# Kernel optimization log

Hardware: AMD Instinct MI355X
Metric: run time of the kernel (lower is better)

The kernel has to match this reference:

```python
import jax, jax.numpy as jnp
import numpy as np

# Instant-NGP style multi-resolution hash grid (torch-ngp convention)
NUM_LEVELS = 32
LEVEL_DIM = 2
LOG2_T = 19
T = 1 << LOG2_T            # per-level hash table size (power of two)
BASE_RES = 1
PER_LEVEL_SCALE = 2.0
PRIMES = (1, 2654435761, 805459861)  # spatial hash primes (uint32, wraps)
# 8 corner offsets of the unit cube, [8, 3]
OFFSETS_NP = np.array([[(c >> d) & 1 for d in range(3)] for c in range(8)], dtype=np.uint32)


def hash_encode(x, embeddings):
    """x: [N,3] in [0,1); embeddings: [L, T, F] -> [N, L*F]."""
    offsets = jnp.asarray(OFFSETS_NP)                       # [8,3] uint32
    offs_f = offsets.astype(x.dtype)                        # [8,3]
    feats = []
    for l in range(NUM_LEVELS):
        scale = float(np.exp2(l * np.log2(PER_LEVEL_SCALE)) * BASE_RES - 1.0)
        res = int(np.ceil(scale)) + 1
        pos = x * jnp.float32(scale) + 0.5                  # [N,3]
        pos0 = jnp.floor(pos)
        frac = pos - pos0                                   # [N,3] in [0,1)
        pg = pos0.astype(jnp.uint32)                        # [N,3]
        corners = pg[:, None, :] + offsets[None, :, :]      # [N,8,3] uint32
        if res ** 3 <= T:
            # dense (non-colliding) linear index at coarse levels
            r = jnp.uint32(res)
            idx = corners[..., 0] + corners[..., 1] * r + corners[..., 2] * (r * r)
        else:
            # spatial hash: xor of coordinate * prime (uint32 wraparound)
            idx = (corners[..., 0] * jnp.uint32(PRIMES[0])
                   ^ corners[..., 1] * jnp.uint32(PRIMES[1])
                   ^ corners[..., 2] * jnp.uint32(PRIMES[2]))
        idx = (idx & jnp.uint32(T - 1)).astype(jnp.int32)   # [N,8]
        f = embeddings[l][idx]                              # gather -> [N,8,F]
        # trilinear interpolation weights
        w = jnp.prod(jnp.where(offs_f[None] == 1, frac[:, None, :], 1.0 - frac[:, None, :]), axis=-1)  # [N,8]
        feats.append(jnp.sum(f * w[..., None], axis=1))     # [N,F]
    return jnp.concatenate(feats, axis=-1)                  # [N, L*F]


def setup_inputs() -> dict:
    key = jax.random.key(0)
    k = jax.random.split(key, 5)
    N = 1 << 20
    x = jax.random.uniform(k[0], (N, 3), dtype=jnp.float32)
    embeddings = jax.random.normal(k[1], (NUM_LEVELS, T, LEVEL_DIM), dtype=jnp.float32) * 1e-2
    in_dim = NUM_LEVELS * LEVEL_DIM  # 64
    W1 = jax.random.normal(k[2], (in_dim, 128), dtype=jnp.float32) * (1.0 / np.sqrt(in_dim))
    b1 = jnp.zeros((128,), jnp.float32)
    W2 = jax.random.normal(k[3], (128, 128), dtype=jnp.float32) * (1.0 / np.sqrt(128))
    b2 = jnp.zeros((128,), jnp.float32)
    W3 = jax.random.normal(k[4], (128, 1), dtype=jnp.float32) * (1.0 / np.sqrt(128))
    b3 = jnp.zeros((1,), jnp.float32)
    return {"x": x, "embeddings": embeddings, "W1": W1, "b1": b1, "W2": W2, "b2": b2, "W3": W3, "b3": b3}


def reference(x, embeddings, W1, b1, W2, b2, W3, b3):
    h = hash_encode(x, embeddings)                 # [N, 64]
    h = jax.nn.relu(h @ W1 + b1)                   # [N, 128]
    h = jax.nn.relu(h @ W2 + b2)                   # [N, 128]
    return h @ W3 + b3                             # [N, 1]
```

## Files before the change

kernel.cpp:

```cpp
#include <hip/hip_runtime.h>
#include <stdint.h>


#define NLV 32
#define LOG2T 19
#define TSZ (1u << LOG2T)
#define TMASK (TSZ - 1u)
#define PRIME2 2654435761u
#define PRIME3 805459861u

typedef float v2f __attribute__((ext_vector_type(2)));
typedef float f32x4 __attribute__((ext_vector_type(4)));
typedef float f32x4u __attribute__((ext_vector_type(4), aligned(8)));
typedef short bf16x8 __attribute__((ext_vector_type(8)));
typedef uint32_t u32x4 __attribute__((ext_vector_type(4)));
typedef uint32_t u32x2 __attribute__((ext_vector_type(2)));

__device__ __forceinline__ uint32_t pack_bf16(float a, float b) {
  uint32_t ua = __float_as_uint(a), ub = __float_as_uint(b);
  ua = (ua + 0x7fffu + ((ua >> 16) & 1u)) >> 16;
  ub = (ub + 0x7fffu + ((ub >> 16) & 1u)) >> 16;
  return ua | (ub << 16);
}
__device__ __forceinline__ uint16_t bf16_rne(float a) {
  uint32_t u = __float_as_uint(a);
  u = (u + 0x7fffu + ((u >> 16) & 1u)) >> 16;
  return (uint16_t)u;
}

__global__ __launch_bounds__(256) void encode_kernel(
    const float* __restrict__ x, const float* __restrict__ emb,
    uint32_t* __restrict__ feats, int offset, int count, int chunkCap, int bpl)
{
  const int bid = (int)blockIdx.x;
  const int xcd = bid & 7;
  const int j = bid >> 3;
  const int phase = j / bpl;
  const int within = j - phase * bpl;
  const int l = xcd + (phase << 3);

  const float scale = (float)((double)(1ULL << l) - 1.0);
  const uint32_t r = 1u << l, rr = r * r;
  const bool dense = (l <= 6);
  const v2f* __restrict__ embl = (const v2f*)(emb + ((size_t)l << (LOG2T + 1)));

  #pragma unroll
  for (int k = 0; k < 4; ++k) {
    int li = within * 1024 + k * 256 + (int)threadIdx.x;
    if (li < count) {
      int p = offset + li;
      float xv = __builtin_nontemporal_load(&x[3 * p + 0]);
      float yv = __builtin_nontemporal_load(&x[3 * p + 1]);
      float zv = __builtin_nontemporal_load(&x[3 * p + 2]);
      float px = __fadd_rn(__fmul_rn(xv, scale), 0.5f);
      float py = __fadd_rn(__fmul_rn(yv, scale), 0.5f);
      float pz = __fadd_rn(__fmul_rn(zv, scale), 0.5f);
      float bx = floorf(px), by = floorf(py), bz = floorf(pz);
      float fx = __fsub_rn(px, bx), fy = __fsub_rn(py, by), fz = __fsub_rn(pz, bz);
      uint32_t gx = (uint32_t)bx, gy = (uint32_t)by, gz = (uint32_t)bz;
      float wx0 = __fsub_rn(1.0f, fx), wx1 = fx;
      float wy0 = __fsub_rn(1.0f, fy), wy1 = fy;
      float wz0 = __fsub_rn(1.0f, fz), wz1 = fz;

      float f0 = 0.0f, f1 = 0.0f;
      #pragma unroll
      for (int cp = 0; cp < 4; ++cp) {
        uint32_t cy = gy + (uint32_t)(cp & 1);
        uint32_t cz = gz + (uint32_t)(cp >> 1);
        float wyz = __fmul_rn((cp & 1) ? wy1 : wy0, (cp >> 1) ? wz1 : wz0);
        v2f e0, e1;
        if (dense) {
          uint32_t i0 = gx + cy * r + cz * rr;
          f32x4 e2 = *(const f32x4u*)&embl[i0];
          e0[0] = e2.x; e0[1] = e2.y; e1[0] = e2.z; e1[1] = e2.w;
        } else {
          uint32_t h = (cy * PRIME2) ^ (cz * PRIME3);
          uint32_t i0 = (gx ^ h) & TMASK;
          if (!(gx & 1u)) {
            f32x4 e2 = *(const f32x4*)&embl[i0 & ~1u];
            bool odd = (i0 & 1u) != 0u;
            e0[0] = odd ? e2.z : e2.x; e0[1] = odd ? e2.w : e2.y;
            e1[0] = odd ? e2.x : e2.z; e1[1] = odd ? e2.y : e2.w;
          } else {
            uint32_t i1 = ((gx + 1u) ^ h) & TMASK;
            e0 = embl[i0];
            e1 = embl[i1];
          }
        }
        float w0 = __fmul_rn(wx0, wyz), w1 = __fmul_rn(wx1, wyz);
        f0 = fmaf(w0, e0[0], f0); f1 = fmaf(w0, e0[1], f1);
        f0 = fmaf(w1, e1[0], f0); f1 = fmaf(w1, e1[1], f1);
      }
      __builtin_nontemporal_store(pack_bf16(f0, f1),
                                  &feats[(size_t)l * (size_t)chunkCap + li]);
    }
  }
}

__global__ __launch_bounds__(512) void prep_kernel(
    const float* __restrict__ W1, const float* __restrict__ W2,
    uint16_t* __restrict__ wimg)
{
  int i = (int)blockIdx.x * 512 + (int)threadIdx.x;
  if (i < 8192) {
    int k = i >> 7, n = i & 127;
    wimg[(n * 128 + ((k * 2) ^ ((n & 7) << 4))) >> 1] = bf16_rne(W1[i]);
  } else if (i < 24576) {
    int t = i - 8192;
    int k = t >> 7, n = t & 127;
    wimg[(16384 + n * 256 + ((k * 2) ^ ((n & 7) << 4))) >> 1] = bf16_rne(W2[t]);
  }
}

#define MLP_G 64

__global__ __launch_bounds__(256, 1) void mlp_kernel(
    const uint32_t* __restrict__ feats, const uint16_t* __restrict__ wimg,
    const float* __restrict__ b1, const float* __restrict__ b2,
    const float* __restrict__ W3, const float* __restrict__ b3,
    float* __restrict__ out, int offset, int count, int chunkCap, int nGroups)
{
  __shared__ char lds[24576];
  char* xb = lds;
  char* hb = lds + 8192;

  const int tid = (int)threadIdx.x;
  const int lane = tid & 63;
  const int w = tid >> 6;
  const int col = lane & 15;
  const int kh = lane >> 4;
  const char* wbytes = (const char*)wimg;

  bf16x8 w1f[2][8], w2f[4][8];
  #pragma unroll
  for (int nt = 0; nt < 8; ++nt) {
    int n = nt * 16 + col;
    #pragma unroll
    for (int kt = 0; kt < 2; ++kt)
      w1f[kt][nt] = *(const bf16x8*)(wbytes + n * 128 +
                        ((kt * 64 + kh * 16) ^ ((n & 7) << 4)));
    #pragma unroll
    for (int q = 0; q < 4; ++q)
      w2f[q][nt] = *(const bf16x8*)(wbytes + 16384 + n * 256 +
                        ((q * 64 + kh * 16) ^ ((n & 7) << 4)));
  }
  float bias1r[8][4];
  #pragma unroll
  for (int nt = 0; nt < 8; ++nt)
    #pragma unroll
    for (int rg = 0; rg < 4; ++rg)
      bias1r[nt][rg] = b1[nt * 16 + kh * 4 + rg];
  float bias2[8], w3v[8];
  #pragma unroll
  for (int nt = 0; nt < 8; ++nt) {
    bias2[nt] = b2[nt * 16 + col];
    w3v[nt] = W3[nt * 16 + col];
  }
  const float b3v = b3[0];

  const int pp = w * 16 + col;
  const int sp = tid & 63;
  const int sq = tid >> 6;

  int g = (int)blockIdx.x;
  u32x4 xr0, xr1;
  {
    int src = g * MLP_G + sp; if (src >= count) src = 0;
    int pl = sq * 8;
    xr0.x = __builtin_nontemporal_load(&feats[(size_t)(pl + 0) * chunkCap + src]);
    xr0.y = __builtin_nontemporal_load(&feats[(size_t)(pl + 1) * chunkCap + src]);
    xr0.z = __builtin_nontemporal_load(&feats[(size_t)(pl + 2) * chunkCap + src]);
    xr0.w = __builtin_nontemporal_load(&feats[(size_t)(pl + 3) * chunkCap + src]);
    xr1.x = __builtin_nontemporal_load(&feats[(size_t)(pl + 4) * chunkCap + src]);
    xr1.y = __builtin_nontemporal_load(&feats[(size_t)(pl + 5) * chunkCap + src]);
    xr1.z = __builtin_nontemporal_load(&feats[(size_t)(pl + 6) * chunkCap + src]);
    xr1.w = __builtin_nontemporal_load(&feats[(size_t)(pl + 7) * chunkCap + src]);
  }

  for (; g < nGroups; g += (int)gridDim.x) {
    *(u32x4*)(xb + sp * 128 + ((sq * 32 +  0) ^ ((sp & 7) << 4))) = xr0;
    *(u32x4*)(xb + sp * 128 + ((sq * 32 + 16) ^ ((sp & 7) << 4))) = xr1;
    __syncthreads();

    {
      int gn = g + (int)gridDim.x; if (gn >= nGroups) gn = g;
      int src = gn * MLP_G + sp; if (src >= count) src = 0;
      int pl = sq * 8;
      xr0.x = __builtin_nontemporal_load(&feats[(size_t)(pl + 0) * chunkCap + src]);
      xr0.y = __builtin_nontemporal_load(&feats[(size_t)(pl + 1) * chunkCap + src]);
      xr0.z = __builtin_nontemporal_load(&feats[(size_t)(pl + 2) * chunkCap + src]);
      xr0.w = __builtin_nontemporal_load(&feats[(size_t)(pl + 3) * chunkCap + src]);
      xr1.x = __builtin_nontemporal_load(&feats[(size_t)(pl + 4) * chunkCap + src]);
      xr1.y = __builtin_nontemporal_load(&feats[(size_t)(pl + 5) * chunkCap + src]);
      xr1.z = __builtin_nontemporal_load(&feats[(size_t)(pl + 6) * chunkCap + src]);
      xr1.w = __builtin_nontemporal_load(&feats[(size_t)(pl + 7) * chunkCap + src]);
    }

    bf16x8 xa[2];
    #pragma unroll
    for (int kt = 0; kt < 2; ++kt)
      xa[kt] = *(const bf16x8*)(xb + pp * 128 +
                   ((kt * 64 + kh * 16) ^ ((pp & 7) << 4)));
    f32x4 acc[8];
    #pragma unroll
    for (int nt = 0; nt < 8; ++nt) acc[nt] = {0.f, 0.f, 0.f, 0.f};
    #pragma unroll
    for (int kt = 0; kt < 2; ++kt)
      #pragma unroll
      for (int nt = 0; nt < 8; ++nt)
        acc[nt] = __builtin_amdgcn_mfma_f32_16x16x32_bf16(
                      w1f[kt][nt], xa[kt], acc[nt], 0, 0, 0);

    #pragma unroll
    for (int nt = 0; nt < 8; ++nt) {
      uint32_t lo = pack_bf16(fmaxf(acc[nt][0] + bias1r[nt][0], 0.0f),
                              fmaxf(acc[nt][1] + bias1r[nt][1], 0.0f));
      uint32_t hi = pack_bf16(fmaxf(acc[nt][2] + bias1r[nt][2], 0.0f),
                              fmaxf(acc[nt][3] + bias1r[nt][3], 0.0f));
      u32x2 v; v.x = lo; v.y = hi;
      *(u32x2*)(hb + pp * 256 + ((nt * 32 + kh * 8) ^ ((pp & 7) << 4))) = v;
    }
    __syncthreads();

    f32x4 acc2[8];
    #pragma unroll
    for (int nt = 0; nt < 8; ++nt) acc2[nt] = {0.f, 0.f, 0.f, 0.f};
    #pragma unroll
    for (int q = 0; q < 4; ++q) {
      bf16x8 ha = *(const bf16x8*)(hb + pp * 256 +
                      ((q * 64 + kh * 16) ^ ((pp & 7) << 4)));
      #pragma unroll
      for (int nt = 0; nt < 8; ++nt)
        acc2[nt] = __builtin_amdgcn_mfma_f32_16x16x32_bf16(
                       ha, w2f[q][nt], acc2[nt], 0, 0, 0);
    }

    float osum[4] = {0.f, 0.f, 0.f, 0.f};
    #pragma unroll
    for (int nt = 0; nt < 8; ++nt) {
      #pragma unroll
      for (int rg = 0; rg < 4; ++rg)
        osum[rg] = fmaf(fmaxf(acc2[nt][rg] + bias2[nt], 0.0f), w3v[nt], osum[rg]);
    }
    #pragma unroll
    for (int rg = 0; rg < 4; ++rg) {
      osum[rg] += __shfl_xor(osum[rg], 1);
      osum[rg] += __shfl_xor(osum[rg], 2);
      osum[rg] += __shfl_xor(osum[rg], 4);
      osum[rg] += __shfl_xor(osum[rg], 8);
    }
    const int base = g * MLP_G;
    #pragma unroll
    for (int rg = 0; rg < 4; ++rg) {
      if (col == rg) {
        int pr = base + w * 16 + kh * 4 + rg;
        if (pr < count) out[offset + pr] = osum[rg] + b3v;
      }
    }
  }
}

extern "C" void kernel_launch(void* const* d_in, const int* in_sizes, int n_in,
                              void* d_out, int out_size, void* d_ws, size_t ws_size,
                              hipStream_t stream) {
  const float* x   = (const float*)d_in[0];
  const float* emb = (const float*)d_in[1];
  const float* W1  = (const float*)d_in[2];
  const float* b1  = (const float*)d_in[3];
  const float* W2  = (const float*)d_in[4];
  const float* b2  = (const float*)d_in[5];
  const float* W3  = (const float*)d_in[6];
  const float* b3  = (const float*)d_in[7];
  float* out = (float*)d_out;
  const int N = in_sizes[0] / 3;

  uint16_t* wimg = (uint16_t*)d_ws;
  uint32_t* feats = (uint32_t*)((char*)d_ws + 49152);
  const size_t perPoint = (size_t)NLV * sizeof(uint32_t);
  size_t avail = (ws_size > 49152) ? ws_size - 49152 : 0;
  size_t capz = avail / perPoint;
  if (capz > (size_t)N) capz = (size_t)N;
  int cap = (int)capz & ~1023;
  if (cap <= 0) cap = (N < 1024) ? N : 1024;

  prep_kernel<<<48, 512, 0, stream>>>(W1, W2, wimg);

  for (int off = 0; off < N; off += cap) {
    int cnt = (N - off < cap) ? (N - off) : cap;
    int bpl = (cnt + 1023) / 1024;
    encode_kernel<<<32 * bpl, 256, 0, stream>>>(x, emb, feats, off, cnt, cap, bpl);
    int nGroups = (cnt + MLP_G - 1) / MLP_G;
    int nb = nGroups < 2048 ? nGroups : 2048;
    mlp_kernel<<<nb, 256, 0, stream>>>(
        feats, wimg, b1, b2, W3, b3, out, off, cnt, cap, nGroups);
  }
}
```

Baseline: 1.056 ms.

## Fuse hash encoding and MLP into a single per-block kernel

Replaces the separate level-major encode kernel and persistent MLP kernel with one kernel. Each 64-point block computes all 32 level features straight into LDS and then runs the two MFMA layers and the output dot product. This removes the global round trip of the intermediate feature buffer, the chunking loop and one kernel launch. In exchange, the level-major schedule that kept one level's table slice hot in cache is lost, since all levels are now gathered concurrently. Weights are also re-read from memory per block instead of staying in registers across a persistent loop.

```diff
diff --git a/kernel.cpp b/kernel.cpp
--- a/kernel.cpp
+++ b/kernel.cpp
@@ -1,5 +1,6 @@
 #include <hip/hip_runtime.h>
 #include <stdint.h>
+#include <math.h>
 
 
 #define NLV 32
@@ -16,6 +17,8 @@
 typedef uint32_t u32x4 __attribute__((ext_vector_type(4)));
 typedef uint32_t u32x2 __attribute__((ext_vector_type(2)));
 
+struct Scales { float s[NLV]; };
+
 __device__ __forceinline__ uint32_t pack_bf16(float a, float b) {
   uint32_t ua = __float_as_uint(a), ub = __float_as_uint(b);
   ua = (ua + 0x7fffu + ((ua >> 16) & 1u)) >> 16;
@@ -26,75 +29,6 @@
   uint32_t u = __float_as_uint(a);
   u = (u + 0x7fffu + ((u >> 16) & 1u)) >> 16;
   return (uint16_t)u;
-}
-
-__global__ __launch_bounds__(256) void encode_kernel(
-    const float* __restrict__ x, const float* __restrict__ emb,
-    uint32_t* __restrict__ feats, int offset, int count, int chunkCap, int bpl)
-{
-  const int bid = (int)blockIdx.x;
-  const int xcd = bid & 7;
-  const int j = bid >> 3;
-  const int phase = j / bpl;
-  const int within = j - phase * bpl;
-  const int l = xcd + (phase << 3);
-
-  const float scale = (float)((double)(1ULL << l) - 1.0);
-  const uint32_t r = 1u << l, rr = r * r;
-  const bool dense = (l <= 6);
-  const v2f* __restrict__ embl = (const v2f*)(emb + ((size_t)l << (LOG2T + 1)));
-
-  #pragma unroll
-  for (int k = 0; k < 4; ++k) {
-    int li = within * 1024 + k * 256 + (int)threadIdx.x;
-    if (li < count) {
-      int p = offset + li;
-      float xv = __builtin_nontemporal_load(&x[3 * p + 0]);
-      float yv = __builtin_nontemporal_load(&x[3 * p + 1]);
-      float zv = __builtin_nontemporal_load(&x[3 * p + 2]);
-      float px = __fadd_rn(__fmul_rn(xv, scale), 0.5f);
-      float py = __fadd_rn(__fmul_rn(yv, scale), 0.5f);
-      float pz = __fadd_rn(__fmul_rn(zv, scale), 0.5f);
-      float bx = floorf(px), by = floorf(py), bz = floorf(pz);
-      float fx = __fsub_rn(px, bx), fy = __fsub_rn(py, by), fz = __fsub_rn(pz, bz);
-      uint32_t gx = (uint32_t)bx, gy = (uint32_t)by, gz = (uint32_t)bz;
-      float wx0 = __fsub_rn(1.0f, fx), wx1 = fx;
-      float wy0 = __fsub_rn(1.0f, fy), wy1 = fy;
-      float wz0 = __fsub_rn(1.0f, fz), wz1 = fz;
-
-      float f0 = 0.0f, f1 = 0.0f;
-      #pragma unroll
-      for (int cp = 0; cp < 4; ++cp) {
-        uint32_t cy = gy + (uint32_t)(cp & 1);
-        uint32_t cz = gz + (uint32_t)(cp >> 1);
-        float wyz = __fmul_rn((cp & 1) ? wy1 : wy0, (cp >> 1) ? wz1 : wz0);
-        v2f e0, e1;
-        if (dense) {
-          uint32_t i0 = gx + cy * r + cz * rr;
-          f32x4 e2 = *(const f32x4u*)&embl[i0];
-          e0[0] = e2.x; e0[1] = e2.y; e1[0] = e2.z; e1[1] = e2.w;
-        } else {
-          uint32_t h = (cy * PRIME2) ^ (cz * PRIME3);
-          uint32_t i0 = (gx ^ h) & TMASK;
-          if (!(gx & 1u)) {
-            f32x4 e2 = *(const f32x4*)&embl[i0 & ~1u];
-            bool odd = (i0 & 1u) != 0u;
-            e0[0] = odd ? e2.z : e2.x; e0[1] = odd ? e2.w : e2.y;
-            e1[0] = odd ? e2.x : e2.z; e1[1] = odd ? e2.y : e2.w;
-          } else {
-            uint32_t i1 = ((gx + 1u) ^ h) & TMASK;
-            e0 = embl[i0];
-            e1 = embl[i1];
-          }
-        }
-        float w0 = __fmul_rn(wx0, wyz), w1 = __fmul_rn(wx1, wyz);
-        f0 = fmaf(w0, e0[0], f0); f1 = fmaf(w0, e0[1], f1);
-        f0 = fmaf(w1, e1[0], f0); f1 = fmaf(w1, e1[1], f1);
-      }
-      __builtin_nontemporal_store(pack_bf16(f0, f1),
-                                  &feats[(size_t)l * (size_t)chunkCap + li]);
-    }
-  }
 }
 
 __global__ __launch_bounds__(512) void prep_kernel(
@@ -112,150 +46,167 @@
   }
 }
 
-#define MLP_G 64
-
-__global__ __launch_bounds__(256, 1) void mlp_kernel(
-    const uint32_t* __restrict__ feats, const uint16_t* __restrict__ wimg,
+__device__ __forceinline__ uint32_t encode_level(
+    float scale, uint32_t r, bool dense, const v2f* __restrict__ embl,
+    float xv, float yv, float zv)
+{
+  float px = __fadd_rn(__fmul_rn(xv, scale), 0.5f);
+  float py = __fadd_rn(__fmul_rn(yv, scale), 0.5f);
+  float pz = __fadd_rn(__fmul_rn(zv, scale), 0.5f);
+  float bx = floorf(px), by = floorf(py), bz = floorf(pz);
+  float fx = __fsub_rn(px, bx), fy = __fsub_rn(py, by), fz = __fsub_rn(pz, bz);
+  uint32_t gx = (uint32_t)bx, gy = (uint32_t)by, gz = (uint32_t)bz;
+  float wx0 = __fsub_rn(1.0f, fx), wx1 = fx;
+  float wy0 = __fsub_rn(1.0f, fy), wy1 = fy;
+  float wz0 = __fsub_rn(1.0f, fz), wz1 = fz;
+  const uint32_t rr = r * r;
+
+  float f0 = 0.0f, f1 = 0.0f;
+  #pragma unroll
+  for (int cp = 0; cp < 4; ++cp) {
+    uint32_t cy = gy + (uint32_t)(cp & 1);
+    uint32_t cz = gz + (uint32_t)(cp >> 1);
+    float wyz = __fmul_rn((cp & 1) ? wy1 : wy0, (cp >> 1) ? wz1 : wz0);
+    v2f e0, e1;
+    if (dense) {
+      uint32_t i0 = gx + cy * r + cz * rr;
+      f32x4 e2 = *(const f32x4u*)&embl[i0];
+      e0[0] = e2.x; e0[1] = e2.y; e1[0] = e2.z; e1[1] = e2.w;
+    } else {
+      uint32_t h = (cy * PRIME2) ^ (cz * PRIME3);
+      uint32_t i0 = (gx ^ h) & TMASK;
+      if (!(gx & 1u)) {
+        f32x4 e2 = *(const f32x4*)&embl[i0 & ~1u];
+        bool odd = (i0 & 1u) != 0u;
+        e0[0] = odd ? e2.z : e2.x; e0[1] = odd ? e2.w : e2.y;
+        e1[0] = odd ? e2.x : e2.z; e1[1] = odd ? e2.y : e2.w;
+      } else {
+        uint32_t i1 = ((gx + 1u) ^ h) & TMASK;
+        e0 = embl[i0];
+        e1 = embl[i1];
+      }
+    }
+    float w0 = __fmul_rn(wx0, wyz), w1 = __fmul_rn(wx1, wyz);
+    f0 = fmaf(w0, e0[0], f0); f1 = fmaf(w0, e0[1], f1);
+    f0 = fmaf(w1, e1[0], f0); f1 = fmaf(w1, e1[1], f1);
+  }
+  return pack_bf16(f0, f1);
+}
+
+__global__ __launch_bounds__(256) void fused_kernel(
+    const float* __restrict__ x, const float* __restrict__ emb,
+    const uint16_t* __restrict__ wimg,
     const float* __restrict__ b1, const float* __restrict__ b2,
     const float* __restrict__ W3, const float* __restrict__ b3,
-    float* __restrict__ out, int offset, int count, int chunkCap, int nGroups)
+    float* __restrict__ out, int count, Scales sc)
 {
   __shared__ char lds[24576];
   char* xb = lds;
   char* hb = lds + 8192;
 
   const int tid = (int)threadIdx.x;
+  const int sp = tid & 63;
+  const int sq = tid >> 6;
+  const int base = (int)blockIdx.x * 64;
+
+  {
+    int gp = base + sp;
+    int src = (gp < count) ? gp : 0;
+    float xv = x[3 * src + 0], yv = x[3 * src + 1], zv = x[3 * src + 2];
+    const int l0 = __builtin_amdgcn_readfirstlane(sq * 8);
+    uint32_t f[8];
+    #pragma unroll
+    for (int i = 0; i < 8; ++i) {
+      const int l = l0 + i;
+      const float scale = sc.s[l];
+      const uint32_t r = 1u << l;
+      const bool dense = (l <= 6);
+      const v2f* embl = (const v2f*)(emb + ((size_t)l << (LOG2T + 1)));
+      f[i] = encode_level(scale, r, dense, embl, xv, yv, zv);
+    }
+    u32x4 v0, v1;
+    v0.x = f[0]; v0.y = f[1]; v0.z = f[2]; v0.w = f[3];
+    v1.x = f[4]; v1.y = f[5]; v1.z = f[6]; v1.w = f[7];
+    int sw = (sp & 7) << 4;
+    *(u32x4*)(xb + sp * 128 + ((sq * 32 +  0) ^ sw)) = v0;
+    *(u32x4*)(xb + sp * 128 + ((sq * 32 + 16) ^ sw)) = v1;
+  }
+  __syncthreads();
+
   const int lane = tid & 63;
   const int w = tid >> 6;
   const int col = lane & 15;
   const int kh = lane >> 4;
+  const int pp = w * 16 + col;
   const char* wbytes = (const char*)wimg;
 
-  bf16x8 w1f[2][8], w2f[4][8];
+  bf16x8 xa[2];
+  #pragma unroll
+  for (int kt = 0; kt < 2; ++kt)
+    xa[kt] = *(const bf16x8*)(xb + pp * 128 +
+                 ((kt * 64 + kh * 16) ^ ((pp & 7) << 4)));
+  f32x4 acc[8];
+  #pragma unroll
+  for (int nt = 0; nt < 8; ++nt) acc[nt] = {0.f, 0.f, 0.f, 0.f};
+  #pragma unroll
+  for (int kt = 0; kt < 2; ++kt)
+    #pragma unroll
+    for (int nt = 0; nt < 8; ++nt) {
+      int n = nt * 16 + col;
+      bf16x8 wf = *(const bf16x8*)(wbytes + n * 128 +
+                      ((kt * 64 + kh * 16) ^ ((n & 7) << 4)));
+      acc[nt] = __builtin_amdgcn_mfma_f32_16x16x32_bf16(wf, xa[kt], acc[nt], 0, 0, 0);
+    }
+
   #pragma unroll
   for (int nt = 0; nt < 8; ++nt) {
-    int n = nt * 16 + col;
-    #pragma unroll
-    for (int kt = 0; kt < 2; ++kt)
-      w1f[kt][nt] = *(const bf16x8*)(wbytes + n * 128 +
-                        ((kt * 64 + kh * 16) ^ ((n & 7) << 4)));
-    #pragma unroll
-    for (int q = 0; q < 4; ++q)
-      w2f[q][nt] = *(const bf16x8*)(wbytes + 16384 + n * 256 +
-                        ((q * 64 + kh * 16) ^ ((n & 7) << 4)));
-  }
-  float bias1r[8][4];
-  #pragma unroll
-  for (int nt = 0; nt < 8; ++nt)
+    f32x4u bias = *(const f32x4u*)(b1 + nt * 16 + kh * 4);
+    uint32_t lo = pack_bf16(fmaxf(acc[nt][0] + bias.x, 0.0f),
+                            fmaxf(acc[nt][1] + bias.y, 0.0f));
+    uint32_t hi = pack_bf16(fmaxf(acc[nt][2] + bias.z, 0.0f),
+                            fmaxf(acc[nt][3] + bias.w, 0.0f));
+    u32x2 v; v.x = lo; v.y = hi;
+    *(u32x2*)(hb + pp * 256 + ((nt * 32 + kh * 8) ^ ((pp & 7) << 4))) = v;
+  }
+
+  f32x4 acc2[8];
+  #pragma unroll
+  for (int nt = 0; nt < 8; ++nt) acc2[nt] = {0.f, 0.f, 0.f, 0.f};
+  #pragma unroll
+  for (int q = 0; q < 4; ++q) {
+    bf16x8 ha = *(const bf16x8*)(hb + pp * 256 +
+                    ((q * 64 + kh * 16) ^ ((pp & 7) << 4)));
+    #pragma unroll
+    for (int nt = 0; nt < 8; ++nt) {
+      int n = nt * 16 + col;
+      bf16x8 wf = *(const bf16x8*)(wbytes + 16384 + n * 256 +
+                      ((q * 64 + kh * 16) ^ ((n & 7) << 4)));
+      acc2[nt] = __builtin_amdgcn_mfma_f32_16x16x32_bf16(ha, wf, acc2[nt], 0, 0, 0);
+    }
+  }
+
+  float osum[4] = {0.f, 0.f, 0.f, 0.f};
+  #pragma unroll
+  for (int nt = 0; nt < 8; ++nt) {
+    float bias = b2[nt * 16 + col];
+    float w3v = W3[nt * 16 + col];
     #pragma unroll
     for (int rg = 0; rg < 4; ++rg)
-      bias1r[nt][rg] = b1[nt * 16 + kh * 4 + rg];
-  float bias2[8], w3v[8];
-  #pragma unroll
-  for (int nt = 0; nt < 8; ++nt) {
-    bias2[nt] = b2[nt * 16 + col];
-    w3v[nt] = W3[nt * 16 + col];
+      osum[rg] = fmaf(fmaxf(acc2[nt][rg] + bias, 0.0f), w3v, osum[rg]);
+  }
+  #pragma unroll
+  for (int rg = 0; rg < 4; ++rg) {
+    osum[rg] += __shfl_xor(osum[rg], 1);
+    osum[rg] += __shfl_xor(osum[rg], 2);
+    osum[rg] += __shfl_xor(osum[rg], 4);
+    osum[rg] += __shfl_xor(osum[rg], 8);
   }
   const float b3v = b3[0];
-
-  const int pp = w * 16 + col;
-  const int sp = tid & 63;
-  const int sq = tid >> 6;
-
-  int g = (int)blockIdx.x;
-  u32x4 xr0, xr1;
-  {
-    int src = g * MLP_G + sp; if (src >= count) src = 0;
-    int pl = sq * 8;
-    xr0.x = __builtin_nontemporal_load(&feats[(size_t)(pl + 0) * chunkCap + src]);
-    xr0.y = __builtin_nontemporal_load(&feats[(size_t)(pl + 1) * chunkCap + src]);
-    xr0.z = __builtin_nontemporal_load(&feats[(size_t)(pl + 2) * chunkCap + src]);
-    xr0.w = __builtin_nontemporal_load(&feats[(size_t)(pl + 3) * chunkCap + src]);
-    xr1.x = __builtin_nontemporal_load(&feats[(size_t)(pl + 4) * chunkCap + src]);
-    xr1.y = __builtin_nontemporal_load(&feats[(size_t)(pl + 5) * chunkCap + src]);
-    xr1.z = __builtin_nontemporal_load(&feats[(size_t)(pl + 6) * chunkCap + src]);
-    xr1.w = __builtin_nontemporal_load(&feats[(size_t)(pl + 7) * chunkCap + src]);
-  }
-
-  for (; g < nGroups; g += (int)gridDim.x) {
-    *(u32x4*)(xb + sp * 128 + ((sq * 32 +  0) ^ ((sp & 7) << 4))) = xr0;
-    *(u32x4*)(xb + sp * 128 + ((sq * 32 + 16) ^ ((sp & 7) << 4))) = xr1;
-    __syncthreads();
-
-    {
-      int gn = g + (int)gridDim.x; if (gn >= nGroups) gn = g;
-      int src = gn * MLP_G + sp; if (src >= count) src = 0;
-      int pl = sq * 8;
-      xr0.x = __builtin_nontemporal_load(&feats[(size_t)(pl + 0) * chunkCap + src]);
-      xr0.y = __builtin_nontemporal_load(&feats[(size_t)(pl + 1) * chunkCap + src]);
-      xr0.z = __builtin_nontemporal_load(&feats[(size_t)(pl + 2) * chunkCap + src]);
-      xr0.w = __builtin_nontemporal_load(&feats[(size_t)(pl + 3) * chunkCap + src]);
-      xr1.x = __builtin_nontemporal_load(&feats[(size_t)(pl + 4) * chunkCap + src]);
-      xr1.y = __builtin_nontemporal_load(&feats[(size_t)(pl + 5) * chunkCap + src]);
-      xr1.z = __builtin_nontemporal_load(&feats[(size_t)(pl + 6) * chunkCap + src]);
-      xr1.w = __builtin_nontemporal_load(&feats[(size_t)(pl + 7) * chunkCap + src]);
-    }
-
-    bf16x8 xa[2];
-    #pragma unroll
-    for (int kt = 0; kt < 2; ++kt)
-      xa[kt] = *(const bf16x8*)(xb + pp * 128 +
-                   ((kt * 64 + kh * 16) ^ ((pp & 7) << 4)));
-    f32x4 acc[8];
-    #pragma unroll
-    for (int nt = 0; nt < 8; ++nt) acc[nt] = {0.f, 0.f, 0.f, 0.f};
-    #pragma unroll
-    for (int kt = 0; kt < 2; ++kt)
-      #pragma unroll
-      for (int nt = 0; nt < 8; ++nt)
-        acc[nt] = __builtin_amdgcn_mfma_f32_16x16x32_bf16(
-                      w1f[kt][nt], xa[kt], acc[nt], 0, 0, 0);
-
-    #pragma unroll
-    for (int nt = 0; nt < 8; ++nt) {
-      uint32_t lo = pack_bf16(fmaxf(acc[nt][0] + bias1r[nt][0], 0.0f),
-                              fmaxf(acc[nt][1] + bias1r[nt][1], 0.0f));
-      uint32_t hi = pack_bf16(fmaxf(acc[nt][2] + bias1r[nt][2], 0.0f),
-                              fmaxf(acc[nt][3] + bias1r[nt][3], 0.0f));
-      u32x2 v; v.x = lo; v.y = hi;
-      *(u32x2*)(hb + pp * 256 + ((nt * 32 + kh * 8) ^ ((pp & 7) << 4))) = v;
-    }
-    __syncthreads();
-
-    f32x4 acc2[8];
-    #pragma unroll
-    for (int nt = 0; nt < 8; ++nt) acc2[nt] = {0.f, 0.f, 0.f, 0.f};
-    #pragma unroll
-    for (int q = 0; q < 4; ++q) {
-      bf16x8 ha = *(const bf16x8*)(hb + pp * 256 +
-                      ((q * 64 + kh * 16) ^ ((pp & 7) << 4)));
-      #pragma unroll
-      for (int nt = 0; nt < 8; ++nt)
-        acc2[nt] = __builtin_amdgcn_mfma_f32_16x16x32_bf16(
-                       ha, w2f[q][nt], acc2[nt], 0, 0, 0);
-    }
-
-    float osum[4] = {0.f, 0.f, 0.f, 0.f};
-    #pragma unroll
-    for (int nt = 0; nt < 8; ++nt) {
-      #pragma unroll
-      for (int rg = 0; rg < 4; ++rg)
-        osum[rg] = fmaf(fmaxf(acc2[nt][rg] + bias2[nt], 0.0f), w3v[nt], osum[rg]);
-    }
-    #pragma unroll
-    for (int rg = 0; rg < 4; ++rg) {
-      osum[rg] += __shfl_xor(osum[rg], 1);
-      osum[rg] += __shfl_xor(osum[rg], 2);
-      osum[rg] += __shfl_xor(osum[rg], 4);
-      osum[rg] += __shfl_xor(osum[rg], 8);
-    }
-    const int base = g * MLP_G;
-    #pragma unroll
-    for (int rg = 0; rg < 4; ++rg) {
-      if (col == rg) {
-        int pr = base + w * 16 + kh * 4 + rg;
-        if (pr < count) out[offset + pr] = osum[rg] + b3v;
-      }
+  #pragma unroll
+  for (int rg = 0; rg < 4; ++rg) {
+    if (col == rg) {
+      int pr = base + w * 16 + kh * 4 + rg;
+      if (pr < count) out[pr] = osum[rg] + b3v;
     }
   }
 }
@@ -275,23 +226,12 @@
   const int N = in_sizes[0] / 3;
 
   uint16_t* wimg = (uint16_t*)d_ws;
-  uint32_t* feats = (uint32_t*)((char*)d_ws + 49152);
-  const size_t perPoint = (size_t)NLV * sizeof(uint32_t);
-  size_t avail = (ws_size > 49152) ? ws_size - 49152 : 0;
-  size_t capz = avail / perPoint;
-  if (capz > (size_t)N) capz = (size_t)N;
-  int cap = (int)capz & ~1023;
-  if (cap <= 0) cap = (N < 1024) ? N : 1024;
+
+  Scales sc;
+  for (int l = 0; l < NLV; ++l)
+    sc.s[l] = (float)(exp2((double)l) - 1.0);
 
   prep_kernel<<<48, 512, 0, stream>>>(W1, W2, wimg);
-
-  for (int off = 0; off < N; off += cap) {
-    int cnt = (N - off < cap) ? (N - off) : cap;
-    int bpl = (cnt + 1023) / 1024;
-    encode_kernel<<<32 * bpl, 256, 0, stream>>>(x, emb, feats, off, cnt, cap, bpl);
-    int nGroups = (cnt + MLP_G - 1) / MLP_G;
-    int nb = nGroups < 2048 ? nGroups : 2048;
-    mlp_kernel<<<nb, 256, 0, stream>>>(
-        feats, wimg, b1, b2, W3, b3, out, off, cnt, cap, nGroups);
-  }
-}
+  fused_kernel<<<(N + 63) / 64, 256, 0, stream>>>(
+      x, emb, wimg, b1, b2, W3, b3, out, N, sc);
+}
```

Result: slower. 1.926 ms (+82.4%).
